# Kernel optimization log

Hardware: AMD Instinct MI355X
Metric: run time of the kernel (lower is better)

The kernel has to match this reference:

```python
import jax, jax.numpy as jnp
import numpy as np

# Model hyperparameters (match init_kwargs)
J, L, A, A_PRIME = 5, 4, 4, 1
M = N = 128
C = 1
NB = 2
DELTA_J, DELTA_L = J, L
MASK_ANGLES = 4
SHIFT_R = 4  # radius (pixels) of directional correlation shifts
EPS = 1e-6


def _pair_indices():
    """Static (i1, i2) indices into the flattened [C*J*L*A] coefficient axis
    for cross-scale/angle correlation pairs: j1 <= j2 <= j1+delta_j,
    circular |l1-l2| <= delta_l, a1 in [0,A), a2 in [0,A_prime)."""
    i1, i2 = [], []
    flat = lambda c, j, l, a: ((c * J + j) * L + l) * A + a
    for c in range(C):
        for j1 in range(J):
            for j2 in range(j1, min(j1 + DELTA_J, J - 1) + 1):
                for l1 in range(L):
                    for l2 in range(L):
                        dl = min((l1 - l2) % L, (l2 - l1) % L)
                        if dl > DELTA_L:
                            continue
                        for a1 in range(A):
                            for a2 in range(A_PRIME):
                                i1.append(flat(c, j1, l1, a1))
                                i2.append(flat(c, j2, l2, a2))
    return np.asarray(i1, np.int32), np.asarray(i2, np.int32)


def _shifts():
    """Zero shift plus MASK_ANGLES directional shifts at radius SHIFT_R."""
    sh = [(0, 0)]
    for s in range(MASK_ANGLES):
        th = np.pi * s / MASK_ANGLES
        sh.append((int(round(SHIFT_R * np.cos(th))), int(round(SHIFT_R * np.sin(th)))))
    return sh


def _highpass_filters():
    """Angular-sector highpass masks in Fourier space: |k| > pi/2 split into
    MASK_ANGLES orientation sectors (angle folded to [0, pi))."""
    kx = 2 * np.pi * np.fft.fftfreq(M)[:, None]
    ky = 2 * np.pi * np.fft.fftfreq(N)[None, :]
    r = np.sqrt(kx ** 2 + ky ** 2)
    th = np.mod(np.arctan2(ky, kx), np.pi)
    h = []
    for s in range(MASK_ANGLES):
        lo, hi = np.pi * s / MASK_ANGLES, np.pi * (s + 1) / MASK_ANGLES
        h.append(((r > np.pi / 2) & (th >= lo) & (th < hi)).astype(np.float32))
    return np.stack(h)  # [MASK_ANGLES, M, N]


def setup_inputs() -> dict:
    key = jax.random.key(0)
    k = jax.random.split(key, 5)
    return {
        "x": jax.random.normal(k[0], (NB, C, M, N), jnp.float32),
        "hatpsi_re": jax.random.normal(k[1], (C, J, L, A, M, N), jnp.float32),
        "hatpsi_im": jax.random.normal(k[2], (C, J, L, A, M, N), jnp.float32),
        "hatphi_re": jax.random.normal(k[3], (M, N), jnp.float32),
        "hatphi_im": jax.random.normal(k[4], (M, N), jnp.float32),
    }


def reference(x, hatpsi_re, hatpsi_im, hatphi_re, hatphi_im):
    nb = x.shape[0]
    # --- WaveConvLayer: FFT wavelet convolution ---
    hatx = jnp.fft.fft2(x)  # [nb, C, M, N] complex
    hatpsi = hatpsi_re + 1j * hatpsi_im  # [C, J, L, A, M, N]
    xpsi = jnp.fft.ifft2(hatx[:, :, None, None, None] * hatpsi[None])  # [nb,C,J,L,A,M,N]
    # --- ReluCenterLayer: ReLU of real part, spatially centered, L2-normalized ---
    y = jax.nn.relu(xpsi.real)
    y = y - y.mean((-2, -1), keepdims=True)
    y = y / (jnp.sqrt((y * y).mean((-2, -1), keepdims=True)) + EPS)
    yf = y.reshape(nb, C * J * L * A, M, N)
    # --- CorrLayer: shifted cross-correlations over pair list ---
    i1, i2 = _pair_indices()
    a1 = yf[:, i1].reshape(nb, -1, M * N)  # [nb, P, M*N]
    a2 = yf[:, i2]                          # [nb, P, M, N]
    corrs = []
    for (dx, dy) in _shifts():  # small fixed set of shifts
        a2r = jnp.roll(a2, (dx, dy), axis=(-2, -1)).reshape(nb, -1, M * N)
        corrs.append(jnp.einsum('npx,npx->np', a1, a2r) / (M * N))
    xcorr = jnp.concatenate(corrs, axis=1)  # [nb, P * n_shifts]
    # --- LowpassLayer: phi-filtered moments (mean, mean-square) ---
    hatphi = hatphi_re + 1j * hatphi_im
    xlow_map = jnp.fft.ifft2(hatx * hatphi).real  # [nb, C, M, N]
    xlow = jnp.stack([xlow_map.mean((-2, -1)), (xlow_map ** 2).mean((-2, -1))], axis=-1)  # [nb,C,2]
    # --- HighpassLayer: per-sector highpass energy (Parseval) ---
    hhigh = jnp.asarray(_highpass_filters())  # [MASK_ANGLES, M, N]
    xhigh = (jnp.abs(hatx[:, :, None] * hhigh) ** 2).mean((-2, -1)) / (M * N)  # [nb,C,MASK_ANGLES]
    return jnp.concatenate([xcorr, xlow.reshape(nb, -1), xhigh.reshape(nb, -1)], axis=1)
```

## Files before the change

kernel.cpp:

```cpp
#include <hip/hip_runtime.h>
#include <math.h>

#define NB 2
#define NMAPS 81
#define NPSI 80
#define PIXELS 16384
#define OUT_STRIDE 4806

constexpr double PI_D = 3.14159265358979323846;

__device__ inline float2 cmulf(float2 a, float2 b) {
  return make_float2(a.x * b.x - a.y * b.y, a.x * b.y + a.y * b.x);
}

template <int CTRL>
__device__ inline float dppf(float v) {
  return __int_as_float(
      __builtin_amdgcn_update_dpp(0, __float_as_int(v), CTRL, 0xf, 0xf, true));
}

__device__ inline float shx(float v, const int mask) {
  if (mask == 1) return dppf<0xB1>(v);
  if (mask == 2) return dppf<0x4E>(v);
  if (mask == 8) return dppf<0x128>(v);
  if (mask == 32) {
    auto r = __builtin_amdgcn_permlane32_swap(__float_as_uint(v),
                                              __float_as_uint(v), false, false);
    return __uint_as_float((threadIdx.x & 32) ? r[0] : r[1]);
  }
  return __shfl_xor(v, mask);
}

__device__ inline float wred64(float v) {
  int x;
  x = __builtin_amdgcn_update_dpp(0, __float_as_int(v), 0x111, 0xf, 0xf, true); v += __int_as_float(x);
  x = __builtin_amdgcn_update_dpp(0, __float_as_int(v), 0x112, 0xf, 0xf, true); v += __int_as_float(x);
  x = __builtin_amdgcn_update_dpp(0, __float_as_int(v), 0x114, 0xf, 0xf, true); v += __int_as_float(x);
  x = __builtin_amdgcn_update_dpp(0, __float_as_int(v), 0x118, 0xf, 0xf, true); v += __int_as_float(x);
  x = __builtin_amdgcn_update_dpp(0, __float_as_int(v), 0x142, 0xa, 0xf, true); v += __int_as_float(x);
  x = __builtin_amdgcn_update_dpp(0, __float_as_int(v), 0x143, 0xc, 0xf, true); v += __int_as_float(x);
  return __int_as_float(__builtin_amdgcn_readlane(__float_as_int(v), 63));
}


__global__ __launch_bounds__(128) void k_fft_rows(const float* __restrict__ x,
                                                  float2* __restrict__ tx,
                                                  int* __restrict__ sector) {
  const int tid = threadIdx.x;
  const int blkid = blockIdx.x;
  if (blkid >= NB * 128) {
    int idx = (blkid - NB * 128) * 128 + tid;
    int i = idx >> 7, j = idx & 127;
    double fx = (double)(i < 64 ? i : i - 128) / 128.0;
    double fy = (double)(j < 64 ? j : j - 128) / 128.0;
    double kx = (2.0 * PI_D) * fx;
    double ky = (2.0 * PI_D) * fy;
    double r2 = kx * kx + ky * ky;
    const double h = PI_D / 2.0;
    int s = -1;
    if (r2 > h * h) {
      double th = atan2(ky, kx);
      th = fmod(th, PI_D);
      if (th < 0.0) th += PI_D;
      if (th < PI_D * 0.25) s = 0;
      else if (th < PI_D * 0.5) s = 1;
      else if (th < PI_D * 0.75) s = 2;
      else if (th < PI_D) s = 3;
    }
    sector[idx] = s;
    return;
  }
  __shared__ float row[128];
  __shared__ float2 wt[128];
  const int m = blkid & 127;
  const int b = blkid >> 7;
  {
    double ang = -(2.0 * PI_D / 128.0) * (double)tid;
    wt[tid] = make_float2((float)cos(ang), (float)sin(ang));
  }
  row[tid] = x[(b << 14) + (m << 7) + tid];
  __syncthreads();
  float ar = 0.f, ai = 0.f;
  int idx = 0;
  const int v = tid;
#pragma unroll 8
  for (int n = 0; n < 128; ++n) {
    float xv = row[n];
    float2 w = wt[idx];
    ar = fmaf(xv, w.x, ar);
    ai = fmaf(xv, w.y, ai);
    idx = (idx + v) & 127;
  }
  tx[(b << 14) + (m << 7) + tid] = make_float2(ar, ai);
}

__global__ __launch_bounds__(128) void k_fft_cols(const float2* __restrict__ tx,
                                                  float2* __restrict__ hatx) {
  __shared__ float2 col[128];
  __shared__ float2 wt[128];
  const int tid = threadIdx.x;
  const int v = blockIdx.x & 127;
  const int b = blockIdx.x >> 7;
  {
    double ang = -(2.0 * PI_D / 128.0) * (double)tid;
    wt[tid] = make_float2((float)cos(ang), (float)sin(ang));
  }
  col[tid] = tx[(b << 14) + (tid << 7) + v];
  __syncthreads();
  float ar = 0.f, ai = 0.f;
  int idx = 0;
  const int u = tid;
#pragma unroll 8
  for (int mm = 0; mm < 128; ++mm) {
    float2 z = col[mm];
    float2 w = wt[idx];
    ar += z.x * w.x - z.y * w.y;
    ai += z.x * w.y + z.y * w.x;
    idx = (idx + u) & 127;
  }
  hatx[(b << 14) + (tid << 7) + v] = make_float2(ar, ai);
}


#define BFLY(z)                                     \
  {                                                 \
    float tx_ = shx((z).x, mask);                   \
    float ty_ = shx((z).y, mask);                   \
    float ax_ = fmaf(s, (z).x, tx_);                \
    float ay_ = fmaf(s, (z).y, ty_);                \
    (z).x = ax_ * we.x - ay_ * we.y;                \
    (z).y = ax_ * we.y + ay_ * we.x;                \
  }

__device__ inline void fft128_inv(float2& z0, float2& z1, float2& z2, float2& z3,
                                  const float2* __restrict__ wt, int l) {
  {
    float2 w = wt[l];
    float2 a0 = make_float2(z0.x + z1.x, z0.y + z1.y);
    float2 d0 = make_float2(z0.x - z1.x, z0.y - z1.y);
    z0 = a0;
    z1 = cmulf(d0, w);
    float2 a1 = make_float2(z2.x + z3.x, z2.y + z3.y);
    float2 d1 = make_float2(z2.x - z3.x, z2.y - z3.y);
    z2 = a1;
    z3 = cmulf(d1, w);
  }
#pragma unroll
  for (int mask = 32; mask >= 1; mask >>= 1) {
    float2 w = wt[(l & (mask - 1)) * (64 / mask)];
    const bool up = (l & mask) != 0;
    const float s = up ? -1.f : 1.f;
    const float2 we = up ? w : make_float2(1.f, 0.f);
    BFLY(z0);
    BFLY(z1);
    BFLY(z2);
    BFLY(z3);
  }
}


__global__ __launch_bounds__(1024) void k_ifft2d(
    const float2* __restrict__ hatx,
    const float* __restrict__ psi_re, const float* __restrict__ psi_im,
    const float* __restrict__ phi_re, const float* __restrict__ phi_im,
    float* __restrict__ y, float2* __restrict__ meaninv,
    float* __restrict__ out) {
  __shared__ float2 Tsh[128 * 129];
  __shared__ float2 wt[64];
  __shared__ float2 red16[16];
  const int tid = threadIdx.x;
  const int l = tid & 63;
  const int w = tid >> 6;
  const int mf = blockIdx.x;
  const int b = mf / NMAPS;
  const int f = mf - b * NMAPS;
  if (tid < 64) {
    double ang = (2.0 * PI_D / 128.0) * (double)tid;
    wt[tid] = make_float2((float)cos(ang), (float)sin(ang));
  }
  __syncthreads();
  const float2* hb2 = hatx + (b << 14);
  const float* fre = (f < NPSI) ? psi_re + ((size_t)f << 14) : phi_re;
  const float* fim = (f < NPSI) ? psi_im + ((size_t)f << 14) : phi_im;
  {
    const int o0 = (w << 1) << 7;
    float2 hA0 = hb2[o0 + l],       hA1 = hb2[o0 + l + 64];
    float2 hB0 = hb2[o0 + 128 + l], hB1 = hb2[o0 + 128 + l + 64];
    float fa0r = fre[o0 + l],            fa0i = fim[o0 + l];
    float fa1r = fre[o0 + l + 64],       fa1i = fim[o0 + l + 64];
    float fb0r = fre[o0 + 128 + l],      fb0i = fim[o0 + 128 + l];
    float fb1r = fre[o0 + 128 + l + 64], fb1i = fim[o0 + 128 + l + 64];
#pragma unroll
    for (int r = 0; r < 4; ++r) {
      const int uA = r * 32 + (w << 1);
      float2 nhA0, nhA1, nhB0, nhB1;
      float nfa0r, nfa0i, nfa1r, nfa1i, nfb0r, nfb0i, nfb1r, nfb1i;
      if (r < 3) {
        const int o = ((r + 1) * 32 + (w << 1)) << 7;
        nhA0 = hb2[o + l];       nhA1 = hb2[o + l + 64];
        nhB0 = hb2[o + 128 + l]; nhB1 = hb2[o + 128 + l + 64];
        nfa0r = fre[o + l];            nfa0i = fim[o + l];
        nfa1r = fre[o + l + 64];       nfa1i = fim[o + l + 64];
        nfb0r = fre[o + 128 + l];      nfb0i = fim[o + 128 + l];
        nfb1r = fre[o + 128 + l + 64]; nfb1i = fim[o + 128 + l + 64];
      }
      float2 zA0 = cmulf(hA0, make_float2(fa0r, fa0i));
      float2 zA1 = cmulf(hA1, make_float2(fa1r, fa1i));
      float2 zB0 = cmulf(hB0, make_float2(fb0r, fb0i));
      float2 zB1 = cmulf(hB1, make_float2(fb1r, fb1i));
      fft128_inv(zA0, zA1, zB0, zB1, wt, l);
      Tsh[l * 129 + uA] = zA0;
      Tsh[(l + 64) * 129 + uA] = zA1;
      Tsh[l * 129 + uA + 1] = zB0;
      Tsh[(l + 64) * 129 + uA + 1] = zB1;
      if (r < 3) {
        hA0 = nhA0; hA1 = nhA1; hB0 = nhB0; hB1 = nhB1;
        fa0r = nfa0r; fa0i = nfa0i; fa1r = nfa1r; fa1i = nfa1i;
        fb0r = nfb0r; fb0i = nfb0i; fb1r = nfb1r; fb1i = nfb1i;
      }
    }
  }
  __syncthreads();
  float s1 = 0.f, s2 = 0.f;
  float* yb = y + ((size_t)(b * NPSI + f) << 14);
  const int m2 = __brev(l) >> 26;
  const int um  = (128 - l) & 127;
  const int um2 = (64 - l) & 127;
  for (int r = 0; r < 2; ++r) {
    const int q0 = r * 64 + (w << 2);
    float2 zA0, zA1, zB0, zB1;
    {
      const float2* C0 = &Tsh[(q0    ) * 129];
      const float2* C1 = &Tsh[(q0 + 1) * 129];
      float2 a0 = C0[l], a0m = C0[um], a1 = C0[l + 64], a1m = C0[um2];
      float2 b0 = C1[l], b0m = C1[um], b1 = C1[l + 64], b1m = C1[um2];
      zA0 = make_float2(0.5f * (a0.x + a0m.x) - 0.5f * (b0.y - b0m.y),
                        0.5f * (a0.y - a0m.y) + 0.5f * (b0.x + b0m.x));
      zA1 = make_float2(0.5f * (a1.x + a1m.x) - 0.5f * (b1.y - b1m.y),
                        0.5f * (a1.y - a1m.y) + 0.5f * (b1.x + b1m.x));
      const float2* C2 = &Tsh[(q0 + 2) * 129];
      const float2* C3 = &Tsh[(q0 + 3) * 129];
      float2 c0 = C2[l], c0m = C2[um], c1 = C2[l + 64], c1m = C2[um2];
      float2 d0 = C3[l], d0m = C3[um], d1 = C3[l + 64], d1m = C3[um2];
      zB0 = make_float2(0.5f * (c0.x + c0m.x) - 0.5f * (d0.y - d0m.y),
                        0.5f * (c0.y - c0m.y) + 0.5f * (d0.x + d0m.x));
      zB1 = make_float2(0.5f * (c1.x + c1m.x) - 0.5f * (d1.y - d1m.y),
                        0.5f * (c1.y - c1m.y) + 0.5f * (d1.x + d1m.x));
    }
    fft128_inv(zA0, zA1, zB0, zB1, wt, l);
    const float sc = 1.f / 16384.f;
    const int nA0 = __brev(q0) >> 25;
    float xA00 = zA0.x * sc, xA01 = zA0.y * sc;
    float xA10 = zA1.x * sc, xA11 = zA1.y * sc;
    float xB00 = zB0.x * sc, xB01 = zB0.y * sc;
    float xB10 = zB1.x * sc, xB11 = zB1.y * sc;
    if (f < NPSI) {
      xA00 = fmaxf(xA00, 0.f); xA01 = fmaxf(xA01, 0.f);
      xA10 = fmaxf(xA10, 0.f); xA11 = fmaxf(xA11, 0.f);
      xB00 = fmaxf(xB00, 0.f); xB01 = fmaxf(xB01, 0.f);
      xB10 = fmaxf(xB10, 0.f); xB11 = fmaxf(xB11, 0.f);
      *(float2*)(yb + ((nA0     ) << 7) + (m2 << 1)) = make_float2(xA00, xA10);
      *(float2*)(yb + ((nA0 + 64) << 7) + (m2 << 1)) = make_float2(xA01, xA11);
      *(float2*)(yb + ((nA0 + 32) << 7) + (m2 << 1)) = make_float2(xB00, xB10);
      *(float2*)(yb + ((nA0 + 96) << 7) + (m2 << 1)) = make_float2(xB01, xB11);
    }
    s1 += xA00 + xA01 + xA10 + xA11 + xB00 + xB01 + xB10 + xB11;
    s2 += xA00 * xA00 + xA01 * xA01 + xA10 * xA10 + xA11 * xA11 +
          xB00 * xB00 + xB01 * xB01 + xB10 * xB10 + xB11 * xB11;
  }
  float t1 = wred64(s1), t2 = wred64(s2);
  if (l == 0) red16[w] = make_float2(t1, t2);
  __syncthreads();
  if (w == 0) {
    float2 p = (l < 16) ? red16[l] : make_float2(0.f, 0.f);
    float S1 = wred64(p.x), S2 = wred64(p.y);
    if (l == 0) {
      float mean = S1 * (1.f / 16384.f);
      float msq  = S2 * (1.f / 16384.f);
      if (f < NPSI) {
        float var = fmaxf(msq - mean * mean, 0.f);
        meaninv[b * NPSI + f] = make_float2(mean, 1.f / (sqrtf(var) + 1e-6f));
      } else {
        out[b * OUT_STRIDE + 4800] = mean;
        out[b * OUT_STRIDE + 4801] = msq;
      }
    }
  }
}

__global__ __launch_bounds__(256) void k_corrtail(
    const float* __restrict__ y, const float2* __restrict__ meaninv,
    const float2* __restrict__ hatx, const int* __restrict__ sector,
    float* __restrict__ out) {
  const int tid = threadIdx.x;
  const int l = tid & 63;
  const int w = tid >> 6;
  const int work = ((blockIdx.x & 7) * 61) + (blockIdx.x >> 3);
  if (work >= NB * 240) {
    const int b = work - NB * 240;
    if (b >= NB) return;
    __shared__ float red[4][4];
    float a0 = 0, a1 = 0, a2 = 0, a3 = 0;
    for (int k = tid; k < PIXELS; k += 256) {
      float2 hx = hatx[(b << 14) + k];
      float mag = hx.x * hx.x + hx.y * hx.y;
      int s = sector[k];
      if (s == 0) a0 += mag;
      else if (s == 1) a1 += mag;
      else if (s == 2) a2 += mag;
      else if (s == 3) a3 += mag;
    }
    a0 = wred64(a0); a1 = wred64(a1); a2 = wred64(a2); a3 = wred64(a3);
    if (l == 0) { red[w][0] = a0; red[w][1] = a1; red[w][2] = a2; red[w][3] = a3; }
    __syncthreads();
    if (tid < 4) {
      float tot = red[0][tid] + red[1][tid] + red[2][tid] + red[3][tid];
      out[b * OUT_STRIDE + 4802 + tid] = tot * (1.f / (16384.f * 16384.f));
    }
    return;
  }
  __shared__ float s2m[128 * 132];
  __shared__ float redb[4 * 20];
  __shared__ float2 mi[5];
  const int b = work / 240;
  const int r_ = work - b * 240;
  const int jj = r_ >> 4;
  const int l1 = (r_ >> 2) & 3;
  const int l2 = r_ & 3;
  int j1 = 0, rem = jj;
  while (rem >= 5 - j1) { rem -= (5 - j1); ++j1; }
  const int j2 = j1 + rem;
  const int i1b = j1 * 16 + l1 * 4;
  const int i2 = j2 * 16 + l2 * 4;
  if (tid < 4) mi[tid] = meaninv[b * NPSI + i1b + tid];
  else if (tid == 4) mi[4] = meaninv[b * NPSI + i2];
  const float* __restrict__ y1 = y + ((size_t)(b * NPSI + i1b) << 14);
  const float* __restrict__ y2 = y + ((size_t)(b * NPSI + i2) << 14);
  const int r0 = tid >> 5;
  const int c4 = (tid & 31) << 2;
#pragma unroll
  for (int k = 0; k < 16; ++k) {
    int row = k * 8 + r0;
    *(float4*)&s2m[row * 132 + c4] = *(const float4*)&y2[(row << 7) + c4];
  }
  __syncthreads();
  if (tid < 128) {
    *(float4*)&s2m[tid * 132 + 128] = *(const float4*)&s2m[tid * 132];
  }
  __syncthreads();
  const int bm4 = (c4 + 124) & 127;
  float acc[20];
#pragma unroll
  for (int o = 0; o < 20; ++o) acc[o] = 0.f;
#pragma unroll 4
  for (int k = 0; k < 16; ++k) {
    const int r = k * 8 + r0;
    const int rm0 = r * 132;
    const int rm3 = ((r + 125) & 127) * 132;
    const int rm4 = ((r + 124) & 127) * 132;
    float4 q0 = *(const float4*)&s2m[rm0 + c4];
    float4 q1 = *(const float4*)&s2m[rm0 + bm4];
    float4 q3 = *(const float4*)&s2m[rm4 + c4];
    float4 qa = *(const float4*)&s2m[rm3 + bm4];
    float4 qb = *(const float4*)&s2m[rm3 + bm4 + 4];
    float4 qd = *(const float4*)&s2m[rm3 + c4 + 4];
    const float u2x = qa.y, u2y = qa.z, u2z = qa.w, u2w = qb.x;
    const float u4x = qb.w, u4y = qd.x, u4z = qd.y, u4w = qd.z;
#pragma unroll
    for (int m = 0; m < 4; ++m) {
      float4 v = *(const float4*)&y1[(m << 14) + (r << 7) + c4];
      acc[m*5+0] = fmaf(v.w,q0.w,fmaf(v.z,q0.z,fmaf(v.y,q0.y,fmaf(v.x,q0.x,acc[m*5+0]))));
      acc[m*5+1] = fmaf(v.w,q1.w,fmaf(v.z,q1.z,fmaf(v.y,q1.y,fmaf(v.x,q1.x,acc[m*5+1]))));
      acc[m*5+2] = fmaf(v.w,u2w,fmaf(v.z,u2z,fmaf(v.y,u2y,fmaf(v.x,u2x,acc[m*5+2]))));
      acc[m*5+3] = fmaf(v.w,q3.w,fmaf(v.z,q3.z,fmaf(v.y,q3.y,fmaf(v.x,q3.x,acc[m*5+3]))));
      acc[m*5+4] = fmaf(v.w,u4w,fmaf(v.z,u4z,fmaf(v.y,u4y,fmaf(v.x,u4x,acc[m*5+4]))));
    }
  }
#pragma unroll
  for (int o = 0; o < 20; ++o) {
    float tot = wred64(acc[o]);
    if (l == 0) redb[w * 20 + o] = tot;
  }
  __syncthreads();
  if (tid < 20) {
    int m = tid / 5, s = tid - m * 5;
    float tot = redb[tid] + redb[20 + tid] + redb[40 + tid] + redb[60 + tid];
    float2 m1 = mi[m], m2 = mi[4];
    float c = m1.y * m2.y * (tot * (1.f / 16384.f) - m1.x * m2.x);
    int p = jj * 64 + l1 * 16 + l2 * 4 + m;
    out[b * OUT_STRIDE + s * 960 + p] = c;
  }
}

extern "C" void kernel_launch(void* const* d_in, const int* in_sizes, int n_in,
                              void* d_out, int out_size, void* d_ws, size_t ws_size,
                              hipStream_t stream) {
  (void)in_sizes; (void)n_in; (void)out_size; (void)ws_size;
  const float* x      = (const float*)d_in[0];
  const float* psi_re = (const float*)d_in[1];
  const float* psi_im = (const float*)d_in[2];
  const float* phi_re = (const float*)d_in[3];
  const float* phi_im = (const float*)d_in[4];
  float* out = (float*)d_out;
  char* ws = (char*)d_ws;

  constexpr size_t TX_BYTES   = (size_t)NB * PIXELS * sizeof(float2);
  constexpr size_t HATX_OFF   = TX_BYTES;
  constexpr size_t HATX_BYTES = (size_t)NB * PIXELS * sizeof(float2);
  constexpr size_t Y_OFF      = HATX_OFF + HATX_BYTES;
  constexpr size_t Y_BYTES    = (size_t)NB * NPSI * PIXELS * sizeof(float);
  constexpr size_t MI_OFF     = Y_OFF + Y_BYTES;
  constexpr size_t MI_BYTES   = (size_t)NB * NPSI * sizeof(float2);
  constexpr size_t SEC_OFF    = MI_OFF + MI_BYTES;

  float2* tx       = (float2*)(ws);
  float2* hatx     = (float2*)(ws + HATX_OFF);
  float*  y        = (float*)(ws + Y_OFF);
  float2* meaninv  = (float2*)(ws + MI_OFF);
  int*    sector   = (int*)(ws + SEC_OFF);

  k_fft_rows<<<NB * 128 + 128, 128, 0, stream>>>(x, tx, sector);
  k_fft_cols<<<NB * 128, 128, 0, stream>>>(tx, hatx);
  k_ifft2d<<<NB * NMAPS, 1024, 0, stream>>>(hatx, psi_re, psi_im, phi_re, phi_im,
                                            y, meaninv, out);
  k_corrtail<<<488, 256, 0, stream>>>(y, meaninv, hatx, sector, out);
}
```

Baseline: 56.45 us.

## Split fused 2D inverse FFT into row and column kernels for more parallelism

Replaces the single 1024-thread-per-map inverse FFT kernel with separate row and column kernels using many small blocks. Row-pass results go through a global intermediate buffer. Per-block partial sums replace the in-kernel mean/std reduction, which moves into the correlation kernel. This raises occupancy on a GPU with many compute units, at the cost of extra global memory traffic and one extra launch.

```diff
diff --git a/kernel.cpp b/kernel.cpp
--- a/kernel.cpp
+++ b/kernel.cpp
@@ -121,7 +121,6 @@
   hatx[(b << 14) + (tid << 7) + v] = make_float2(ar, ai);
 }
 
-
 #define BFLY(z)                                     \
   {                                                 \
     float tx_ = shx((z).x, mask);                   \
@@ -159,87 +158,106 @@
 }
 
 
-__global__ __launch_bounds__(1024) void k_ifft2d(
+__global__ __launch_bounds__(256) void k_ifft_rows(
     const float2* __restrict__ hatx,
     const float* __restrict__ psi_re, const float* __restrict__ psi_im,
     const float* __restrict__ phi_re, const float* __restrict__ phi_im,
-    float* __restrict__ y, float2* __restrict__ meaninv,
-    float* __restrict__ out) {
-  __shared__ float2 Tsh[128 * 129];
+    float2* __restrict__ t) {
   __shared__ float2 wt[64];
-  __shared__ float2 red16[16];
+  __shared__ float2 stg[128 * 9];
   const int tid = threadIdx.x;
   const int l = tid & 63;
   const int w = tid >> 6;
-  const int mf = blockIdx.x;
+  const int blk = blockIdx.x;
+  const int mf = blk >> 4;
+  const int u0 = (blk & 15) << 3;
   const int b = mf / NMAPS;
   const int f = mf - b * NMAPS;
   if (tid < 64) {
     double ang = (2.0 * PI_D / 128.0) * (double)tid;
     wt[tid] = make_float2((float)cos(ang), (float)sin(ang));
   }
-  __syncthreads();
-  const float2* hb2 = hatx + (b << 14);
-  const float* fre = (f < NPSI) ? psi_re + ((size_t)f << 14) : phi_re;
-  const float* fim = (f < NPSI) ? psi_im + ((size_t)f << 14) : phi_im;
+  const int uA = u0 + (w << 1);
+  float2 zA0, zA1, zB0, zB1;
   {
-    const int o0 = (w << 1) << 7;
-    float2 hA0 = hb2[o0 + l],       hA1 = hb2[o0 + l + 64];
-    float2 hB0 = hb2[o0 + 128 + l], hB1 = hb2[o0 + 128 + l + 64];
-    float fa0r = fre[o0 + l],            fa0i = fim[o0 + l];
-    float fa1r = fre[o0 + l + 64],       fa1i = fim[o0 + l + 64];
-    float fb0r = fre[o0 + 128 + l],      fb0i = fim[o0 + 128 + l];
-    float fb1r = fre[o0 + 128 + l + 64], fb1i = fim[o0 + 128 + l + 64];
-#pragma unroll
-    for (int r = 0; r < 4; ++r) {
-      const int uA = r * 32 + (w << 1);
-      float2 nhA0, nhA1, nhB0, nhB1;
-      float nfa0r, nfa0i, nfa1r, nfa1i, nfb0r, nfb0i, nfb1r, nfb1i;
-      if (r < 3) {
-        const int o = ((r + 1) * 32 + (w << 1)) << 7;
-        nhA0 = hb2[o + l];       nhA1 = hb2[o + l + 64];
-        nhB0 = hb2[o + 128 + l]; nhB1 = hb2[o + 128 + l + 64];
-        nfa0r = fre[o + l];            nfa0i = fim[o + l];
-        nfa1r = fre[o + l + 64];       nfa1i = fim[o + l + 64];
-        nfb0r = fre[o + 128 + l];      nfb0i = fim[o + 128 + l];
-        nfb1r = fre[o + 128 + l + 64]; nfb1i = fim[o + 128 + l + 64];
-      }
-      float2 zA0 = cmulf(hA0, make_float2(fa0r, fa0i));
-      float2 zA1 = cmulf(hA1, make_float2(fa1r, fa1i));
-      float2 zB0 = cmulf(hB0, make_float2(fb0r, fb0i));
-      float2 zB1 = cmulf(hB1, make_float2(fb1r, fb1i));
-      fft128_inv(zA0, zA1, zB0, zB1, wt, l);
-      Tsh[l * 129 + uA] = zA0;
-      Tsh[(l + 64) * 129 + uA] = zA1;
-      Tsh[l * 129 + uA + 1] = zB0;
-      Tsh[(l + 64) * 129 + uA + 1] = zB1;
-      if (r < 3) {
-        hA0 = nhA0; hA1 = nhA1; hB0 = nhB0; hB1 = nhB1;
-        fa0r = nfa0r; fa0i = nfa0i; fa1r = nfa1r; fa1i = nfa1i;
-        fb0r = nfb0r; fb0i = nfb0i; fb1r = nfb1r; fb1i = nfb1i;
-      }
-    }
-  }
-  __syncthreads();
-  float s1 = 0.f, s2 = 0.f;
+    const float2* hA = hatx + (b << 14) + (uA << 7);
+    float2 hA0 = hA[l], hA1 = hA[l + 64];
+    float2 hB0 = hA[128 + l], hB1 = hA[128 + l + 64];
+    float2 fA0, fA1, fB0, fB1;
+    if (f < NPSI) {
+      int poA = (f << 14) + (uA << 7);
+      fA0 = make_float2(psi_re[poA + l], psi_im[poA + l]);
+      fA1 = make_float2(psi_re[poA + l + 64], psi_im[poA + l + 64]);
+      fB0 = make_float2(psi_re[poA + 128 + l], psi_im[poA + 128 + l]);
+      fB1 = make_float2(psi_re[poA + 128 + l + 64], psi_im[poA + 128 + l + 64]);
+    } else {
+      int poA = (uA << 7);
+      fA0 = make_float2(phi_re[poA + l], phi_im[poA + l]);
+      fA1 = make_float2(phi_re[poA + l + 64], phi_im[poA + l + 64]);
+      fB0 = make_float2(phi_re[poA + 128 + l], phi_im[poA + 128 + l]);
+      fB1 = make_float2(phi_re[poA + 128 + l + 64], phi_im[poA + 128 + l + 64]);
+    }
+    zA0 = cmulf(hA0, fA0);
+    zA1 = cmulf(hA1, fA1);
+    zB0 = cmulf(hB0, fB0);
+    zB1 = cmulf(hB1, fB1);
+  }
+  __syncthreads();
+  fft128_inv(zA0, zA1, zB0, zB1, wt, l);
+  const int sA = w << 1, sB = sA + 1;
+  stg[l * 9 + sA] = zA0;
+  stg[(l + 64) * 9 + sA] = zA1;
+  stg[l * 9 + sB] = zB0;
+  stg[(l + 64) * 9 + sB] = zB1;
+  __syncthreads();
+  float2* tb = t + (mf << 14);
+#pragma unroll
+  for (int kk = 0; kk < 4; ++kk) {
+    int k = tid + kk * 256;
+    int p = k >> 3, uu = k & 7;
+    tb[(p << 7) + u0 + uu] = stg[p * 9 + uu];
+  }
+}
+
+
+__global__ __launch_bounds__(256) void k_ifft_cols(
+    const float2* __restrict__ t, float* __restrict__ y,
+    float2* __restrict__ partials) {
+  __shared__ float2 wt[64];
+  const int tid = threadIdx.x;
+  const int l = tid & 63;
+  const int w = tid >> 6;
+  const int blk = blockIdx.x;
+  const int mf = blk >> 2;
+  const int pr = blk & 3;
+  const int b = mf / NMAPS;
+  const int f = mf - b * NMAPS;
+  if (tid < 64) {
+    double ang = (2.0 * PI_D / 128.0) * (double)tid;
+    wt[tid] = make_float2((float)cos(ang), (float)sin(ang));
+  }
+  __syncthreads();
+  const float2* tb = t + (mf << 14);
   float* yb = y + ((size_t)(b * NPSI + f) << 14);
   const int m2 = __brev(l) >> 26;
   const int um  = (128 - l) & 127;
   const int um2 = (64 - l) & 127;
-  for (int r = 0; r < 2; ++r) {
-    const int q0 = r * 64 + (w << 2);
+  float s1 = 0.f, s2 = 0.f;
+#pragma unroll
+  for (int pp = 0; pp < 2; ++pp) {
+    const int q0 = pr * 32 + pp * 16 + (w << 2);
     float2 zA0, zA1, zB0, zB1;
     {
-      const float2* C0 = &Tsh[(q0    ) * 129];
-      const float2* C1 = &Tsh[(q0 + 1) * 129];
+      const float2* C0 = tb + ((q0    ) << 7);
+      const float2* C1 = tb + ((q0 + 1) << 7);
       float2 a0 = C0[l], a0m = C0[um], a1 = C0[l + 64], a1m = C0[um2];
       float2 b0 = C1[l], b0m = C1[um], b1 = C1[l + 64], b1m = C1[um2];
       zA0 = make_float2(0.5f * (a0.x + a0m.x) - 0.5f * (b0.y - b0m.y),
                         0.5f * (a0.y - a0m.y) + 0.5f * (b0.x + b0m.x));
       zA1 = make_float2(0.5f * (a1.x + a1m.x) - 0.5f * (b1.y - b1m.y),
                         0.5f * (a1.y - a1m.y) + 0.5f * (b1.x + b1m.x));
-      const float2* C2 = &Tsh[(q0 + 2) * 129];
-      const float2* C3 = &Tsh[(q0 + 3) * 129];
+      const float2* C2 = tb + ((q0 + 2) << 7);
+      const float2* C3 = tb + ((q0 + 3) << 7);
       float2 c0 = C2[l], c0m = C2[um], c1 = C2[l + 64], c1m = C2[um2];
       float2 d0 = C3[l], d0m = C3[um], d1 = C3[l + 64], d1m = C3[um2];
       zB0 = make_float2(0.5f * (c0.x + c0m.x) - 0.5f * (d0.y - d0m.y),
@@ -269,27 +287,11 @@
           xB00 * xB00 + xB01 * xB01 + xB10 * xB10 + xB11 * xB11;
   }
   float t1 = wred64(s1), t2 = wred64(s2);
-  if (l == 0) red16[w] = make_float2(t1, t2);
-  __syncthreads();
-  if (w == 0) {
-    float2 p = (l < 16) ? red16[l] : make_float2(0.f, 0.f);
-    float S1 = wred64(p.x), S2 = wred64(p.y);
-    if (l == 0) {
-      float mean = S1 * (1.f / 16384.f);
-      float msq  = S2 * (1.f / 16384.f);
-      if (f < NPSI) {
-        float var = fmaxf(msq - mean * mean, 0.f);
-        meaninv[b * NPSI + f] = make_float2(mean, 1.f / (sqrtf(var) + 1e-6f));
-      } else {
-        out[b * OUT_STRIDE + 4800] = mean;
-        out[b * OUT_STRIDE + 4801] = msq;
-      }
-    }
-  }
+  if (l == 0) partials[mf * 16 + pr * 4 + w] = make_float2(t1, t2);
 }
 
 __global__ __launch_bounds__(256) void k_corrtail(
-    const float* __restrict__ y, const float2* __restrict__ meaninv,
+    const float* __restrict__ y, const float2* __restrict__ partials,
     const float2* __restrict__ hatx, const int* __restrict__ sector,
     float* __restrict__ out) {
   const int tid = threadIdx.x;
@@ -316,11 +318,19 @@
     if (tid < 4) {
       float tot = red[0][tid] + red[1][tid] + red[2][tid] + red[3][tid];
       out[b * OUT_STRIDE + 4802 + tid] = tot * (1.f / (16384.f * 16384.f));
+    } else if (tid == 8) {
+      float S1 = 0.f, S2 = 0.f;
+      const float2* pp = partials + (size_t)(b * NMAPS + NPSI) * 16;
+#pragma unroll
+      for (int i = 0; i < 16; ++i) { S1 += pp[i].x; S2 += pp[i].y; }
+      out[b * OUT_STRIDE + 4800] = S1 * (1.f / 16384.f);
+      out[b * OUT_STRIDE + 4801] = S2 * (1.f / 16384.f);
     }
     return;
   }
   __shared__ float s2m[128 * 132];
   __shared__ float redb[4 * 20];
+  __shared__ float2 sp[80];
   __shared__ float2 mi[5];
   const int b = work / 240;
   const int r_ = work - b * 240;
@@ -332,8 +342,20 @@
   const int j2 = j1 + rem;
   const int i1b = j1 * 16 + l1 * 4;
   const int i2 = j2 * 16 + l2 * 4;
-  if (tid < 4) mi[tid] = meaninv[b * NPSI + i1b + tid];
-  else if (tid == 4) mi[4] = meaninv[b * NPSI + i2];
+  if (tid < 80) {
+    int mm = tid >> 4, pi = tid & 15;
+    int fidx = (mm < 4) ? (i1b + mm) : i2;
+    sp[tid] = partials[(size_t)(b * NMAPS + fidx) * 16 + pi];
+  }
+  __syncthreads();
+  if (tid < 5) {
+    float S1 = 0.f, S2 = 0.f;
+#pragma unroll
+    for (int i = 0; i < 16; ++i) { S1 += sp[tid * 16 + i].x; S2 += sp[tid * 16 + i].y; }
+    float mean = S1 * (1.f / 16384.f);
+    float var = fmaxf(S2 * (1.f / 16384.f) - mean * mean, 0.f);
+    mi[tid] = make_float2(mean, 1.f / (sqrtf(var) + 1e-6f));
+  }
   const float* __restrict__ y1 = y + ((size_t)(b * NPSI + i1b) << 14);
   const float* __restrict__ y2 = y + ((size_t)(b * NPSI + i2) << 14);
   const int r0 = tid >> 5;
@@ -407,21 +429,25 @@
   constexpr size_t TX_BYTES   = (size_t)NB * PIXELS * sizeof(float2);
   constexpr size_t HATX_OFF   = TX_BYTES;
   constexpr size_t HATX_BYTES = (size_t)NB * PIXELS * sizeof(float2);
-  constexpr size_t Y_OFF      = HATX_OFF + HATX_BYTES;
+  constexpr size_t T_OFF      = HATX_OFF + HATX_BYTES;
+  constexpr size_t T_BYTES    = (size_t)NB * NMAPS * PIXELS * sizeof(float2);
+  constexpr size_t Y_OFF      = T_OFF + T_BYTES;
   constexpr size_t Y_BYTES    = (size_t)NB * NPSI * PIXELS * sizeof(float);
-  constexpr size_t MI_OFF     = Y_OFF + Y_BYTES;
-  constexpr size_t MI_BYTES   = (size_t)NB * NPSI * sizeof(float2);
-  constexpr size_t SEC_OFF    = MI_OFF + MI_BYTES;
+  constexpr size_t SEC_OFF    = Y_OFF + Y_BYTES;
+  constexpr size_t SEC_BYTES  = (size_t)PIXELS * sizeof(int);
+  constexpr size_t PART_OFF   = SEC_OFF + SEC_BYTES;
 
   float2* tx       = (float2*)(ws);
   float2* hatx     = (float2*)(ws + HATX_OFF);
+  float2* t        = (float2*)(ws + T_OFF);
   float*  y        = (float*)(ws + Y_OFF);
-  float2* meaninv  = (float2*)(ws + MI_OFF);
   int*    sector   = (int*)(ws + SEC_OFF);
+  float2* partials = (float2*)(ws + PART_OFF);
 
   k_fft_rows<<<NB * 128 + 128, 128, 0, stream>>>(x, tx, sector);
   k_fft_cols<<<NB * 128, 128, 0, stream>>>(tx, hatx);
-  k_ifft2d<<<NB * NMAPS, 1024, 0, stream>>>(hatx, psi_re, psi_im, phi_re, phi_im,
-                                            y, meaninv, out);
-  k_corrtail<<<488, 256, 0, stream>>>(y, meaninv, hatx, sector, out);
-}
+  k_ifft_rows<<<NB * NMAPS * 16, 256, 0, stream>>>(hatx, psi_re, psi_im,
+                                                   phi_re, phi_im, t);
+  k_ifft_cols<<<NB * NMAPS * 4, 256, 0, stream>>>(t, y, partials);
+  k_corrtail<<<488, 256, 0, stream>>>(y, partials, hatx, sector, out);
+}
```

New measurement: 60.52 us. +7.2%, slower.
